# Kernel tuning notes

Measured on AMD Instinct MI355X. Metric: run time of the kernel, lower is better.

## Reference

```python
import jax, jax.numpy as jnp
import numpy as np

N_BINS = 10


def setup_inputs() -> dict:
    key = jax.random.key(0)
    k1, k2 = jax.random.split(key)
    N, C = 131072, 1000
    logits = jax.random.normal(k1, (N, C), dtype=jnp.float32)
    labels = jax.random.randint(k2, (N,), 0, C, dtype=jnp.int64)
    return {"logits": logits, "labels": labels}


def reference(logits, labels):
    N, C = logits.shape
    probs = jax.nn.softmax(logits, axis=1)  # [N, C]
    # bin b covers (b/n_bins, (b+1)/n_bins]: value v -> ceil(v*n_bins)-1, clipped
    bins = jnp.clip(jnp.ceil(probs * N_BINS).astype(jnp.int32) - 1, 0, N_BINS - 1)
    valid = probs > 0.0  # torch uses gt(lower): exactly-0 confidences fall in no bin
    # flatten (class, bin) -> single segment id
    seg = (bins + jnp.arange(C, dtype=jnp.int32)[None, :] * N_BINS).reshape(-1)
    w = valid.reshape(-1).astype(probs.dtype)
    cnt = jax.ops.segment_sum(w, seg, num_segments=C * N_BINS)
    sum_conf = jax.ops.segment_sum((probs * valid).reshape(-1), seg, num_segments=C * N_BINS)
    correct = (labels[:, None] == jnp.arange(C, dtype=labels.dtype)[None, :]) & valid
    sum_acc = jax.ops.segment_sum(correct.reshape(-1).astype(probs.dtype), seg, num_segments=C * N_BINS)
    prop_in_bin = cnt / N
    safe_cnt = jnp.where(cnt > 0, cnt, 1.0)
    gap = jnp.abs(sum_conf / safe_cnt - sum_acc / safe_cnt)
    per_bin = jnp.where(cnt > 0, gap * prop_in_bin, 0.0)  # [C*n_bins]
    per_class_sce = per_bin.reshape(C, N_BINS).sum(axis=1)  # [C]
    return jnp.mean(per_class_sce).reshape(-1)
```

## Files before the change

### kernel.cpp

```cpp
#include <hip/hip_runtime.h>
#include <math.h>

#define CLS 1000
#define NB 10
#define HIST (CLS * NB)
#define TPB 256
#define WPB (TPB / 64)
#define GRID 1024

#define WAITVM(n) asm volatile("s_waitcnt vmcnt(" #n ")" ::: "memory")

__global__ void ece_init_kernel(float* conf_g, unsigned* acc_g) {
    int i = blockIdx.x * blockDim.x + threadIdx.x;
    if (i < HIST) {
        conf_g[i] = 0.0f;
        acc_g[i]  = 0u;
    }
}

__device__ __forceinline__ void stage_row(const float* __restrict__ logits,
                                          int row, float* dst, int lane, bool last)
{
    const float* src = logits + (size_t)row * CLS + 4 * lane;
    #pragma unroll
    for (int k = 0; k < 3; ++k) {
        __builtin_amdgcn_global_load_lds(
            (const __attribute__((address_space(1))) unsigned int*)(src + 256 * k),
            (__attribute__((address_space(3))) unsigned int*)(dst + 256 * k),
            16, 0, 0);
    }
    if (!last) {
        __builtin_amdgcn_global_load_lds(
            (const __attribute__((address_space(1))) unsigned int*)(src + 768),
            (__attribute__((address_space(3))) unsigned int*)(dst + 768),
            16, 0, 0);
    }
}

__global__ __launch_bounds__(TPB, 4) void ece_hist_kernel(
    const float* __restrict__ logits, const int* __restrict__ labels,
    float* __restrict__ conf_g, unsigned* __restrict__ acc_g, int N)
{
    __shared__ float stage_s[WPB * 2 * 1024];
    __shared__ float conf0_s[CLS];
    for (int i = threadIdx.x; i < CLS; i += blockDim.x) conf0_s[i] = 0.0f;
    __syncthreads();

    const int lane = threadIdx.x & 63;
    const int wib  = threadIdx.x >> 6;
    const int gw   = blockIdx.x * WPB + wib;
    const int nw   = GRID * WPB;

    float* slice = &stage_s[wib * 2048];

    float racc[16];
    #pragma unroll
    for (int j = 0; j < 16; ++j) racc[j] = 0.0f;

    int buf = 0;
    if (gw < N) stage_row(logits, gw, slice, lane, gw == N - 1);

    for (int r = gw; r < N; r += nw) {
        const int rn = r + nw;
        if (rn < N) {
            if (rn == N - 1) {
                stage_row(logits, rn, slice + (buf ^ 1) * 1024, lane, true);
                WAITVM(3);
            } else {
                stage_row(logits, rn, slice + (buf ^ 1) * 1024, lane, false);
                WAITVM(4);
            }
        } else {
            WAITVM(0);
        }
        __builtin_amdgcn_sched_barrier(0);

        float* bufp = slice + buf * 1024;
        const int lab = labels[r];
        const bool lastrow = (r == N - 1);

        float p[16];
        #pragma unroll
        for (int k = 0; k < 4; ++k) {
            float4 v;
            if (k == 3 && lastrow) {
                const float* src = logits + (size_t)r * CLS;
                const int cb = 768 + 4 * lane;
                v.x = (cb + 0 < CLS) ? src[cb + 0] : 0.0f;
                v.y = (cb + 1 < CLS) ? src[cb + 1] : 0.0f;
                v.z = (cb + 2 < CLS) ? src[cb + 2] : 0.0f;
                v.w = (cb + 3 < CLS) ? src[cb + 3] : 0.0f;
            } else {
                v = *(const float4*)&bufp[k * 256 + 4 * lane];
            }
            p[4 * k + 0] = v.x; p[4 * k + 1] = v.y;
            p[4 * k + 2] = v.z; p[4 * k + 3] = v.w;
        }

        #pragma unroll
        for (int j = 0; j < 16; ++j) {
            float e = __expf(p[j]);
            if (j >= 12) {
                int c = 768 + 4 * lane + (j & 3);
                e = (c < CLS) ? e : 0.0f;
            }
            p[j] = e;
        }
        float t0 = (p[0] + p[1]) + (p[2] + p[3]);
        float t1 = (p[4] + p[5]) + (p[6] + p[7]);
        float t2 = (p[8] + p[9]) + (p[10] + p[11]);
        float t3 = (p[12] + p[13]) + (p[14] + p[15]);
        float s  = (t0 + t1) + (t2 + t3);
        #pragma unroll
        for (int off = 32; off; off >>= 1) s += __shfl_xor(s, off);
        const float inv = 1.0f / s;

        float qmax = 0.0f;
        #pragma unroll
        for (int j = 0; j < 16; ++j) {
            float q = p[j] * inv;
            p[j] = q;
            qmax = fmaxf(qmax, q);
            racc[j] += (q <= 0.1f) ? q : 0.0f;
        }
        if (__any(qmax > 0.1f)) {
            #pragma unroll
            for (int j = 0; j < 16; ++j) {
                float q = p[j];
                if (q > 0.1f) {
                    int c  = 256 * (j >> 2) + 4 * lane + (j & 3);
                    int bb = (int)ceilf(q * (float)NB) - 1;
                    bb = bb < 0 ? 0 : (bb > NB - 1 ? NB - 1 : bb);
                    atomicAdd(&conf_g[bb * CLS + c], q);
                }
            }
        }

        float xl;
        if (lastrow && lab >= 768) xl = logits[(size_t)r * CLS + lab];
        else                       xl = bufp[lab];
        float ql = __expf(xl) * inv;
        if (lane == 0 && ql > 0.0f) {
            int bb = 0;
            if (ql > 0.1f) {
                bb = (int)ceilf(ql * (float)NB) - 1;
                bb = bb > NB - 1 ? NB - 1 : bb;
            }
            atomicAdd(&acc_g[bb * CLS + lab], 1u);
        }

        buf ^= 1;
    }

    #pragma unroll
    for (int j = 0; j < 16; ++j) {
        int c = 256 * (j >> 2) + 4 * lane + (j & 3);
        if (c < CLS && racc[j] != 0.0f) atomicAdd(&conf0_s[c], racc[j]);
    }
    __syncthreads();
    for (int i = threadIdx.x; i < CLS; i += blockDim.x) {
        float v = conf0_s[i];
        if (v != 0.0f) atomicAdd(&conf_g[i], v);
    }
}

__global__ void ece_final_kernel(const float* __restrict__ conf_g,
                                 const unsigned* __restrict__ acc_g,
                                 float* __restrict__ out, int N)
{
    __shared__ double wsum[16];
    double s = 0.0;
    for (int i = threadIdx.x; i < HIST; i += blockDim.x) {
        s += fabs((double)conf_g[i] - (double)acc_g[i]);
    }
    #pragma unroll
    for (int off = 32; off; off >>= 1) s += __shfl_xor(s, off);
    int lane = threadIdx.x & 63, w = threadIdx.x >> 6;
    if (lane == 0) wsum[w] = s;
    __syncthreads();
    if (threadIdx.x == 0) {
        double t = 0.0;
        int nwv = blockDim.x >> 6;
        for (int i = 0; i < nwv; ++i) t += wsum[i];
        out[0] = (float)(t / ((double)N * (double)CLS));
    }
}

extern "C" void kernel_launch(void* const* d_in, const int* in_sizes, int n_in,
                              void* d_out, int out_size, void* d_ws, size_t ws_size,
                              hipStream_t stream) {
    const float* logits = (const float*)d_in[0];
    const int*   labels = (const int*)d_in[1];
    const int N = in_sizes[1];

    float*    conf_g = (float*)d_ws;
    unsigned* acc_g  = (unsigned*)((char*)d_ws + HIST * sizeof(float));
    float*    out    = (float*)d_out;

    ece_init_kernel<<<(HIST + 255) / 256, 256, 0, stream>>>(conf_g, acc_g);
    ece_hist_kernel<<<GRID, TPB, 0, stream>>>(logits, labels, conf_g, acc_g, N);
    ece_final_kernel<<<1, 1024, 0, stream>>>(conf_g, acc_g, out, N);
}
```

Measured before the change: 137.5 us.

## Triple-buffer row staging with overlapped tail load and resize grid

Each wave now uses a three-slot LDS ring and keeps two rows of logits in flight instead of one, so more loads are outstanding to hide memory latency. The fourth chunk of every row is loaded from an offset that ends exactly at column 999, which removes the out-of-bounds special case for the last row and its scalar global reads. The grid drops from 1024 to 768 blocks to match the larger LDS footprint (about 48 KB per block), which means fewer resident blocks per CU. The per-class accumulation buffer now reuses the staging LDS instead of a separate array.

```diff
diff --git a/kernel.cpp b/kernel.cpp
--- a/kernel.cpp
+++ b/kernel.cpp
@@ -6,7 +6,8 @@
 #define HIST (CLS * NB)
 #define TPB 256
 #define WPB (TPB / 64)
-#define GRID 1024
+#define GRID 768
+#define NWAVE (GRID * WPB)
 
 #define WAITVM(n) asm volatile("s_waitcnt vmcnt(" #n ")" ::: "memory")
 
@@ -19,7 +20,7 @@
 }
 
 __device__ __forceinline__ void stage_row(const float* __restrict__ logits,
-                                          int row, float* dst, int lane, bool last)
+                                          int row, float* dst, int lane)
 {
     const float* src = logits + (size_t)row * CLS + 4 * lane;
     #pragma unroll
@@ -29,70 +30,55 @@
             (__attribute__((address_space(3))) unsigned int*)(dst + 256 * k),
             16, 0, 0);
     }
-    if (!last) {
-        __builtin_amdgcn_global_load_lds(
-            (const __attribute__((address_space(1))) unsigned int*)(src + 768),
-            (__attribute__((address_space(3))) unsigned int*)(dst + 768),
-            16, 0, 0);
-    }
+    __builtin_amdgcn_global_load_lds(
+        (const __attribute__((address_space(1))) unsigned int*)(src + 744),
+        (__attribute__((address_space(3))) unsigned int*)(dst + 768),
+        16, 0, 0);
 }
 
 __global__ __launch_bounds__(TPB, 4) void ece_hist_kernel(
     const float* __restrict__ logits, const int* __restrict__ labels,
     float* __restrict__ conf_g, unsigned* __restrict__ acc_g, int N)
 {
-    __shared__ float stage_s[WPB * 2 * 1024];
-    __shared__ float conf0_s[CLS];
-    for (int i = threadIdx.x; i < CLS; i += blockDim.x) conf0_s[i] = 0.0f;
-    __syncthreads();
+    __shared__ float stage_s[WPB * 3 * 1024];
 
     const int lane = threadIdx.x & 63;
     const int wib  = threadIdx.x >> 6;
     const int gw   = blockIdx.x * WPB + wib;
-    const int nw   = GRID * WPB;
+    const int nw   = NWAVE;
 
-    float* slice = &stage_s[wib * 2048];
+    float* slice = &stage_s[wib * 3072];
 
     float racc[16];
     #pragma unroll
     for (int j = 0; j < 16; ++j) racc[j] = 0.0f;
 
-    int buf = 0;
-    if (gw < N) stage_row(logits, gw, slice, lane, gw == N - 1);
+    if (gw < N)      stage_row(logits, gw,      slice,        lane);
+    if (gw + nw < N) stage_row(logits, gw + nw, slice + 1024, lane);
 
+    int cur = 0;
     for (int r = gw; r < N; r += nw) {
-        const int rn = r + nw;
-        if (rn < N) {
-            if (rn == N - 1) {
-                stage_row(logits, rn, slice + (buf ^ 1) * 1024, lane, true);
-                WAITVM(3);
-            } else {
-                stage_row(logits, rn, slice + (buf ^ 1) * 1024, lane, false);
-                WAITVM(4);
-            }
+        const int rn2 = r + 2 * nw;
+        if (rn2 < N) {
+            int b2 = cur + 2; if (b2 >= 3) b2 -= 3;
+            stage_row(logits, rn2, slice + b2 * 1024, lane);
+            WAITVM(8);
+        } else if (r + nw < N) {
+            WAITVM(4);
         } else {
             WAITVM(0);
         }
         __builtin_amdgcn_sched_barrier(0);
 
-        float* bufp = slice + buf * 1024;
+        float* bufp = slice + cur * 1024;
         const int lab = labels[r];
-        const bool lastrow = (r == N - 1);
 
         float p[16];
         #pragma unroll
         for (int k = 0; k < 4; ++k) {
-            float4 v;
-            if (k == 3 && lastrow) {
-                const float* src = logits + (size_t)r * CLS;
-                const int cb = 768 + 4 * lane;
-                v.x = (cb + 0 < CLS) ? src[cb + 0] : 0.0f;
-                v.y = (cb + 1 < CLS) ? src[cb + 1] : 0.0f;
-                v.z = (cb + 2 < CLS) ? src[cb + 2] : 0.0f;
-                v.w = (cb + 3 < CLS) ? src[cb + 3] : 0.0f;
-            } else {
-                v = *(const float4*)&bufp[k * 256 + 4 * lane];
-            }
+            int idx = (k < 3) ? (k * 256 + 4 * lane)
+                              : (792 + 4 * ((lane < 58) ? lane : 0));
+            float4 v = *(const float4*)&bufp[idx];
             p[4 * k + 0] = v.x; p[4 * k + 1] = v.y;
             p[4 * k + 2] = v.z; p[4 * k + 3] = v.w;
         }
@@ -136,9 +122,8 @@
             }
         }
 
-        float xl;
-        if (lastrow && lab >= 768) xl = logits[(size_t)r * CLS + lab];
-        else                       xl = bufp[lab];
+        const int li = (lab >= 768) ? lab + 24 : lab;
+        float xl = bufp[li];
         float ql = __expf(xl) * inv;
         if (lane == 0 && ql > 0.0f) {
             int bb = 0;
@@ -149,17 +134,20 @@
             atomicAdd(&acc_g[bb * CLS + lab], 1u);
         }
 
-        buf ^= 1;
+        cur = (cur + 1 == 3) ? 0 : cur + 1;
     }
 
+    __syncthreads();
+    for (int i = threadIdx.x; i < CLS; i += blockDim.x) stage_s[i] = 0.0f;
+    __syncthreads();
     #pragma unroll
     for (int j = 0; j < 16; ++j) {
         int c = 256 * (j >> 2) + 4 * lane + (j & 3);
-        if (c < CLS && racc[j] != 0.0f) atomicAdd(&conf0_s[c], racc[j]);
+        if (c < CLS && racc[j] != 0.0f) atomicAdd(&stage_s[c], racc[j]);
     }
     __syncthreads();
     for (int i = threadIdx.x; i < CLS; i += blockDim.x) {
-        float v = conf0_s[i];
+        float v = stage_s[i];
         if (v != 0.0f) atomicAdd(&conf_g[i], v);
     }
 }
```

After: 129.2 us (median of 2 runs). 1.06x faster.
